# Performance work log

Measured on AMD Instinct MI355X. Metric: run time of the kernel, lower is better.

Reference implementation:

```python
import jax, jax.numpy as jnp
import numpy as np

# ---- Mamba2 hyperparameters (from init_kwargs + mamba_ssm defaults) ----
D_MODEL = 1024
D_STATE = 64
D_CONV = 4
EXPAND = 2
HEADDIM = 64                       # mamba_ssm default
D_INNER = EXPAND * D_MODEL         # 2048
NHEADS = D_INNER // HEADDIM        # 32
CONV_DIM = D_INNER + 2 * D_STATE   # 2176 (ngroups=1)
D_IN_PROJ = 2 * D_INNER + 2 * D_STATE + NHEADS  # 4256
CHUNK = 64                         # SSD chunk length
EPS = 1e-5


def segsum(x):
    """Stable segment-sum: out[..., i, j] = sum_{k=j+1..i} x[..., k] for i>=j, else -inf."""
    T = x.shape[-1]
    cs = jnp.cumsum(x, axis=-1)
    ss = cs[..., :, None] - cs[..., None, :]
    mask = jnp.tril(jnp.ones((T, T), dtype=bool))
    return jnp.where(mask, ss, -jnp.inf)


def setup_inputs() -> dict:
    key = jax.random.key(0)
    ks = jax.random.split(key, 8)
    x = jax.random.normal(ks[0], (2, 2048, D_MODEL), dtype=jnp.float32)
    ln_w = jnp.ones((D_MODEL,), jnp.float32)
    ln_b = jnp.zeros((D_MODEL,), jnp.float32)
    in_proj_w = jax.random.normal(ks[1], (D_MODEL, D_IN_PROJ), jnp.float32) * 0.02
    conv_w = jax.random.normal(ks[2], (CONV_DIM, D_CONV), jnp.float32) * 0.2
    conv_b = jnp.zeros((CONV_DIM,), jnp.float32)
    dt_bias = jax.random.normal(ks[3], (NHEADS,), jnp.float32) * 0.5
    A_log = jnp.log(jax.random.uniform(ks[4], (NHEADS,), jnp.float32, 1.0, 16.0))
    D = jnp.ones((NHEADS,), jnp.float32)
    norm_w = jnp.ones((D_INNER,), jnp.float32)
    out_proj_w = jax.random.normal(ks[5], (D_INNER, D_MODEL), jnp.float32) * 0.02
    return {"x": x, "ln_w": ln_w, "ln_b": ln_b, "in_proj_w": in_proj_w,
            "conv_w": conv_w, "conv_b": conv_b, "dt_bias": dt_bias,
            "A_log": A_log, "D": D, "norm_w": norm_w, "out_proj_w": out_proj_w}


def reference(x, ln_w, ln_b, in_proj_w, conv_w, conv_b, dt_bias, A_log, D,
              norm_w, out_proj_w):
    b, l, _ = x.shape
    # ---- pre-norm (LayerNorm) ----
    mu = jnp.mean(x, -1, keepdims=True)
    var = jnp.mean((x - mu) ** 2, -1, keepdims=True)
    h = (x - mu) * jax.lax.rsqrt(var + EPS) * ln_w + ln_b

    # ---- input projection & split ----
    zxbcdt = h @ in_proj_w                                   # (b,l,4256)
    z, xBC, dt = jnp.split(zxbcdt, [D_INNER, D_INNER + CONV_DIM], axis=-1)

    # ---- causal depthwise conv1d + SiLU ----
    xp = jnp.pad(xBC, ((0, 0), (D_CONV - 1, 0), (0, 0)))
    xconv = sum(xp[:, k:k + l, :] * conv_w[:, k] for k in range(D_CONV)) + conv_b
    xBC = jax.nn.silu(xconv)
    xs, B, C = jnp.split(xBC, [D_INNER, D_INNER + D_STATE], axis=-1)

    dt = jax.nn.softplus(dt + dt_bias)                       # (b,l,h)
    A = -jnp.exp(A_log)                                      # (h,)
    X = xs.reshape(b, l, NHEADS, HEADDIM)                    # (b,l,h,p)

    # ---- SSD chunked selective scan ----
    c = l // CHUNK
    X_dt = X * dt[..., None]
    A_dt = dt * A                                            # (b,l,h)
    Xc = X_dt.reshape(b, c, CHUNK, NHEADS, HEADDIM)          # (b,c,T,h,p)
    Ac = A_dt.reshape(b, c, CHUNK, NHEADS).transpose(0, 3, 1, 2)  # (b,h,c,T)
    Bc = B.reshape(b, c, CHUNK, D_STATE)                     # (b,c,T,n)
    Cc = C.reshape(b, c, CHUNK, D_STATE)

    A_cs = jnp.cumsum(Ac, axis=-1)                           # (b,h,c,T)
    Lmat = jnp.exp(segsum(Ac))                               # (b,h,c,T,T)
    Y_diag = jnp.einsum("bcln,bcsn,bhcls,bcshp->bclhp", Cc, Bc, Lmat, Xc)

    decay_states = jnp.exp(A_cs[..., -1:] - A_cs)            # (b,h,c,T)
    states = jnp.einsum("bcln,bhcl,bclhp->bchpn", Bc, decay_states, Xc)

    A_last = jnp.pad(A_cs[..., -1], ((0, 0), (0, 0), (1, 0)))
    decay_chunk = jnp.exp(segsum(A_last))                    # (b,h,c+1,c+1)
    states = jnp.concatenate([jnp.zeros_like(states[:, :1]), states], axis=1)
    states = jnp.einsum("bhzc,bchpn->bzhpn", decay_chunk, states)[:, :-1]

    Y_off = jnp.einsum("bcln,bchpn,bhcl->bclhp", Cc, states, jnp.exp(A_cs))
    Y = (Y_diag + Y_off).reshape(b, l, NHEADS, HEADDIM)

    # ---- D skip, gated RMSNorm, output projection ----
    Y = Y + X * D[None, None, :, None]
    y = Y.reshape(b, l, D_INNER)
    y = y * jax.nn.silu(z)
    y = y * jax.lax.rsqrt(jnp.mean(y * y, -1, keepdims=True) + EPS) * norm_w
    out = y @ out_proj_w

    return x + out  # residual
```

## Files before the change

kernel.cpp:

```cpp
#include <hip/hip_runtime.h>
#include <hip/hip_bf16.h>

#define BATCH   2
#define SEQ     2048
#define DMODEL  1024
#define DINNER  2048
#define DSTATE  64
#define NHEADS  32
#define HEADDIM 64
#define CONVDIM 2176
#define DINPROJ 4256
#define NPAD    4352
#define NCHUNK  32
#define EPSF    1e-5f
#define SP      88

typedef __bf16 bf16;
typedef bf16  bf16x8 __attribute__((ext_vector_type(8)));
typedef float f32x4  __attribute__((ext_vector_type(4)));

__device__ __forceinline__ void gll16(const bf16* g, bf16* l) {
    __builtin_amdgcn_global_load_lds(
        (const __attribute__((address_space(1))) void*)g,
        (__attribute__((address_space(3))) void*)l, 16, 0, 0);
}

__global__ __launch_bounds__(256) void ln_kernel(
    const float* __restrict__ x, const float* __restrict__ w,
    const float* __restrict__ bv, bf16* __restrict__ h) {
    int row = blockIdx.x;
    const float* xr = x + (size_t)row * DMODEL;
    bf16* hr = h + (size_t)row * DMODEL;
    int t = threadIdx.x;
    float4 v = ((const float4*)xr)[t];
    float s  = v.x + v.y + v.z + v.w;
    float ss = v.x*v.x + v.y*v.y + v.z*v.z + v.w*v.w;
    for (int o = 32; o > 0; o >>= 1) { s += __shfl_down(s, o); ss += __shfl_down(ss, o); }
    __shared__ float red[2][4];
    int wid = t >> 6, lane = t & 63;
    if (lane == 0) { red[0][wid] = s; red[1][wid] = ss; }
    __syncthreads();
    if (t == 0) {
        float a = 0, b2 = 0;
        for (int i = 0; i < 4; i++) { a += red[0][i]; b2 += red[1][i]; }
        red[0][0] = a; red[1][0] = b2;
    }
    __syncthreads();
    float mean = red[0][0] * (1.f / DMODEL);
    float var  = red[1][0] * (1.f / DMODEL) - mean * mean;
    float rstd = rsqrtf(var + EPSF);
    for (int i = t; i < DMODEL; i += 256)
        hr[i] = (bf16)((xr[i] - mean) * rstd * w[i] + bv[i]);
}

__global__ __launch_bounds__(256) void cvt_w_kernel(
    const float* __restrict__ W, bf16* __restrict__ Bt, int K, int N, int NP) {
    __shared__ float sm[32][33];
    int n0 = blockIdx.x * 32, k0 = blockIdx.y * 32;
    int tx = threadIdx.x & 31, ty = threadIdx.x >> 5;
    for (int i = 0; i < 4; i++) {
        int k = k0 + ty + i * 8, n = n0 + tx;
        sm[ty + i * 8][tx] = (n < N) ? W[(size_t)k * N + n] : 0.f;
    }
    __syncthreads();
    for (int i = 0; i < 4; i++) {
        int n = n0 + ty + i * 8, k = k0 + tx;
        if (n < NP) Bt[(size_t)n * K + k] = (bf16)sm[tx][ty + i * 8];
    }
}

template<int BM, int BN, typename OUT_T>
__global__ __launch_bounds__(256) void gemm_bf16_pipe(
    const bf16* __restrict__ A, const bf16* __restrict__ Bt,
    OUT_T* __restrict__ C, int M, int N, int K,
    const float* __restrict__ resid) {
    constexpr int MR = BM / 32;
    constexpr int NR = BN / 32;
    __shared__ __align__(16) bf16 sA[2][BM * 32];
    __shared__ __align__(16) bf16 sB[2][BN * 32];
    int t = threadIdx.x;
    int lane = t & 63, w = t >> 6;
    int m0 = blockIdx.y * BM, n0 = blockIdx.x * BN;
    int wm = w >> 1, wn = w & 1;
    f32x4 acc[MR][NR] = {};
    int srow = w * 16 + (lane >> 2);
    int scol = (lane & 3) * 8;
    int fr = lane & 15;
    int fc = (lane >> 4) * 8;
    auto stage = [&](int buf, int k0) {
        #pragma unroll
        for (int i = 0; i < BM / 64; i++)
            gll16(&A[(size_t)(m0 + i * 64 + srow) * K + k0 + scol],
                  &sA[buf][(i * 64 + w * 16) * 32]);
        #pragma unroll
        for (int i = 0; i < BN / 64; i++)
            gll16(&Bt[(size_t)(n0 + i * 64 + srow) * K + k0 + scol],
                  &sB[buf][(i * 64 + w * 16) * 32]);
    };
    int nt = K / 32;
    stage(0, 0);
    __syncthreads();
    int cur = 0;
    for (int tt = 0; tt < nt; tt++) {
        if (tt + 1 < nt) stage(cur ^ 1, (tt + 1) * 32);
        bf16x8 af[MR], bfr[NR];
        #pragma unroll
        for (int i = 0; i < MR; i++)
            af[i] = *(const bf16x8*)&sA[cur][(wm * (BM/2) + i * 16 + fr) * 32 + fc];
        #pragma unroll
        for (int j = 0; j < NR; j++)
            bfr[j] = *(const bf16x8*)&sB[cur][(wn * (BN/2) + j * 16 + fr) * 32 + fc];
        #pragma unroll
        for (int i = 0; i < MR; i++)
            #pragma unroll
            for (int j = 0; j < NR; j++)
                acc[i][j] = __builtin_amdgcn_mfma_f32_16x16x32_bf16(
                    af[i], bfr[j], acc[i][j], 0, 0, 0);
        __syncthreads();
        cur ^= 1;
    }
    #pragma unroll
    for (int i = 0; i < MR; i++) {
        #pragma unroll
        for (int j = 0; j < NR; j++) {
            int col = n0 + wn * (BN/2) + j * 16 + (lane & 15);
            #pragma unroll
            for (int r = 0; r < 4; r++) {
                int row = m0 + wm * (BM/2) + i * 16 + (lane >> 4) * 4 + r;
                float v = acc[i][j][r];
                if (resid) v += resid[(size_t)row * N + col];
                C[(size_t)row * N + col] = (OUT_T)v;
            }
        }
    }
}

__global__ __launch_bounds__(256) void conv_kernel(
    const bf16* __restrict__ zx, const float* __restrict__ cw,
    const float* __restrict__ cb, bf16* __restrict__ xs,
    bf16* __restrict__ Bm, bf16* __restrict__ Cm) {
    int idx = blockIdx.x * 256 + threadIdx.x;
    int ch = idx % CONVDIM;
    int bl = idx / CONVDIM;
    int b = bl / SEQ, tt = bl % SEQ;
    float acc = cb[ch];
    #pragma unroll
    for (int k = 0; k < 4; k++) {
        int tp = tt - 3 + k;
        if (tp >= 0)
            acc += (float)zx[(size_t)(b * SEQ + tp) * NPAD + DINNER + ch] * cw[ch * 4 + k];
    }
    float s = acc / (1.f + expf(-acc));
    if (ch < DINNER)              xs[(size_t)bl * DINNER + ch] = (bf16)s;
    else if (ch < DINNER+DSTATE)  Bm[bl * DSTATE + (ch - DINNER)] = (bf16)s;
    else                          Cm[bl * DSTATE + (ch - DINNER - DSTATE)] = (bf16)s;
}

__global__ __launch_bounds__(256) void dt_kernel(
    const bf16* __restrict__ zx, const float* __restrict__ dt_bias,
    float* __restrict__ dtb) {
    int idx = blockIdx.x * 256 + threadIdx.x;
    int hh = idx % NHEADS;
    int bl = idx / NHEADS;
    float v = (float)zx[(size_t)bl * NPAD + (DINNER + CONVDIM) + hh] + dt_bias[hh];
    dtb[idx] = (v > 20.f) ? v : log1pf(expf(v));
}

__global__ __launch_bounds__(256) void ssd_states_kernel(
    const bf16* __restrict__ xs, const bf16* __restrict__ Bm,
    const float* __restrict__ dtb, const float* __restrict__ A_log,
    float* __restrict__ states, float* __restrict__ Acs_g) {
    int blk = blockIdx.x;
    int hh = blk % NHEADS;
    int bc = blk / NHEADS;
    int c = bc % NCHUNK, b = bc / NCHUNK;
    __shared__ __align__(16) bf16 sXT[64 * SP];
    __shared__ __align__(16) bf16 sBT[64 * SP];
    __shared__ float dts[64], acs[64];
    int t = threadIdx.x;
    float Ah = -expf(A_log[hh]);
    if (t < 64) {
        float dv = dtb[(b * SEQ + c * 64 + t) * NHEADS + hh];
        float v = dv * Ah;
        #pragma unroll
        for (int o = 1; o < 64; o <<= 1) {
            float p = __shfl_up(v, o);
            if (t >= o) v += p;
        }
        dts[t] = dv; acs[t] = v;
        Acs_g[((b * NHEADS + hh) * NCHUNK + c) * 64 + t] = v;
    }
    __syncthreads();
    float alast = acs[63];
    {
        int l = t >> 2, c0 = (t & 3) * 16;
        int row = b * SEQ + c * 64 + l;
        float dl = dts[l];
        float wl = expf(alast - acs[l]);
        bf16x8 xv0 = *(const bf16x8*)&xs[(size_t)row * DINNER + hh * 64 + c0];
        bf16x8 xv1 = *(const bf16x8*)&xs[(size_t)row * DINNER + hh * 64 + c0 + 8];
        bf16x8 bv0 = *(const bf16x8*)&Bm[(size_t)row * DSTATE + c0];
        bf16x8 bv1 = *(const bf16x8*)&Bm[(size_t)row * DSTATE + c0 + 8];
        #pragma unroll
        for (int i = 0; i < 8; i++) {
            sXT[(c0 + i) * SP + l]     = (bf16)((float)xv0[i] * dl);
            sXT[(c0 + 8 + i) * SP + l] = (bf16)((float)xv1[i] * dl);
            sBT[(c0 + i) * SP + l]     = (bf16)((float)bv0[i] * wl);
            sBT[(c0 + 8 + i) * SP + l] = (bf16)((float)bv1[i] * wl);
        }
    }
    __syncthreads();
    int lane = t & 63, w = t >> 6;
    int wm = w >> 1, wn = w & 1;
    int fr = lane & 15, fc = (lane >> 4) * 8;
    f32x4 acc[2][2] = {};
    #pragma unroll
    for (int kk = 0; kk < 2; kk++) {
        bf16x8 a[2], bb[2];
        #pragma unroll
        for (int i = 0; i < 2; i++)
            a[i] = *(const bf16x8*)&sXT[(wm * 32 + i * 16 + fr) * SP + kk * 32 + fc];
        #pragma unroll
        for (int j = 0; j < 2; j++)
            bb[j] = *(const bf16x8*)&sBT[(wn * 32 + j * 16 + fr) * SP + kk * 32 + fc];
        #pragma unroll
        for (int i = 0; i < 2; i++)
            #pragma unroll
            for (int j = 0; j < 2; j++)
                acc[i][j] = __builtin_amdgcn_mfma_f32_16x16x32_bf16(
                    a[i], bb[j], acc[i][j], 0, 0, 0);
    }
    float* outp = states + (size_t)blk * 4096;
    #pragma unroll
    for (int i = 0; i < 2; i++)
        #pragma unroll
        for (int j = 0; j < 2; j++)
            #pragma unroll
            for (int r = 0; r < 4; r++)
                outp[(wm*32 + i*16 + (lane>>4)*4 + r) * 64 + wn*32 + j*16 + (lane&15)]
                    = acc[i][j][r];
}

__global__ __launch_bounds__(256) void ssd_scan_kernel(
    float* __restrict__ states, const float* __restrict__ Acs_g) {
    int bid = blockIdx.x;
    int slice = bid & 7, bh = bid >> 3;
    int hh = bh % NHEADS, b = bh / NHEADS;
    int e0 = slice * 512 + threadIdx.x * 2;
    float2 loc[NCHUNK];
    float dec[NCHUNK];
    #pragma unroll
    for (int c = 0; c < NCHUNK; c++) {
        loc[c] = *(const float2*)&states[(size_t)((b*NCHUNK+c)*NHEADS+hh)*4096 + e0];
        dec[c] = expf(Acs_g[((b*NHEADS+hh)*NCHUNK + c)*64 + 63]);
    }
    float2 S = make_float2(0.f, 0.f);
    #pragma unroll
    for (int c = 0; c < NCHUNK; c++) {
        float2 l = loc[c];
        *(float2*)&states[(size_t)((b*NCHUNK+c)*NHEADS+hh)*4096 + e0] = S;
        S.x = dec[c]*S.x + l.x;
        S.y = dec[c]*S.y + l.y;
    }
}

__global__ __launch_bounds__(256) void ssd_out_kernel(
    const bf16* __restrict__ xs, const bf16* __restrict__ Bm,
    const bf16* __restrict__ Cm, const float* __restrict__ dtb,
    const float* __restrict__ states, const float* __restrict__ Acs_g,
    const float* __restrict__ Dv, float* __restrict__ Y) {
    int blk = blockIdx.x;
    int hh = blk % NHEADS;
    int bc = blk / NHEADS;
    int c = bc % NCHUNK, b = bc / NCHUNK;
    __shared__ __align__(16) bf16 sC [64 * SP];
    __shared__ __align__(16) bf16 sBG[64 * SP];
    __shared__ __align__(16) bf16 sXS[64 * SP];
    __shared__ float acs[64], dts[64];
    int t = threadIdx.x;
    float4 sreg[4];
    {
        const float* sp = states + (size_t)blk * 4096 + t * 16;
        #pragma unroll
        for (int i = 0; i < 4; i++) sreg[i] = *(const float4*)&sp[i * 4];
    }
    if (t < 64) {
        acs[t] = Acs_g[((b * NHEADS + hh) * NCHUNK + c) * 64 + t];
        dts[t] = dtb[(b * SEQ + c * 64 + t) * NHEADS + hh];
    }
    {
        int l = t >> 2, c0 = (t & 3) * 16;
        int row = b * SEQ + c * 64 + l;
        *(bf16x8*)&sC[l * SP + c0]      = *(const bf16x8*)&Cm[(size_t)row * DSTATE + c0];
        *(bf16x8*)&sC[l * SP + c0 + 8]  = *(const bf16x8*)&Cm[(size_t)row * DSTATE + c0 + 8];
        *(bf16x8*)&sBG[l * SP + c0]     = *(const bf16x8*)&Bm[(size_t)row * DSTATE + c0];
        *(bf16x8*)&sBG[l * SP + c0 + 8] = *(const bf16x8*)&Bm[(size_t)row * DSTATE + c0 + 8];
        bf16x8 xv0 = *(const bf16x8*)&xs[(size_t)row * DINNER + hh * 64 + c0];
        bf16x8 xv1 = *(const bf16x8*)&xs[(size_t)row * DINNER + hh * 64 + c0 + 8];
        #pragma unroll
        for (int i = 0; i < 8; i++) {
            sXS[(c0 + i) * SP + l]     = xv0[i];
            sXS[(c0 + 8 + i) * SP + l] = xv1[i];
        }
    }
    __syncthreads();
    int lane = t & 63, w = t >> 6;
    int wm = w >> 1, wn = w & 1;
    int fr = lane & 15, fc = (lane >> 4) * 8;
    f32x4 g[2][2] = {};
    #pragma unroll
    for (int kk = 0; kk < 2; kk++) {
        bf16x8 a[2], bb[2];
        #pragma unroll
        for (int i = 0; i < 2; i++)
            a[i] = *(const bf16x8*)&sC[(wm * 32 + i * 16 + fr) * SP + kk * 32 + fc];
        #pragma unroll
        for (int j = 0; j < 2; j++)
            bb[j] = *(const bf16x8*)&sBG[(wn * 32 + j * 16 + fr) * SP + kk * 32 + fc];
        #pragma unroll
        for (int i = 0; i < 2; i++)
            #pragma unroll
            for (int j = 0; j < 2; j++)
                g[i][j] = __builtin_amdgcn_mfma_f32_16x16x32_bf16(a[i], bb[j], g[i][j], 0, 0, 0);
    }
    __syncthreads();
    #pragma unroll
    for (int i = 0; i < 2; i++) {
        #pragma unroll
        for (int j = 0; j < 2; j++) {
            int s = wn * 32 + j * 16 + (lane & 15);
            #pragma unroll
            for (int r = 0; r < 4; r++) {
                int l = wm * 32 + i * 16 + (lane >> 4) * 4 + r;
                float val = (s <= l) ? g[i][j][r] * expf(acs[l] - acs[s]) * dts[s] : 0.f;
                sBG[l * SP + s] = (bf16)val;
            }
        }
    }
    __syncthreads();
    f32x4 yd[2][2] = {};
    #pragma unroll
    for (int kk = 0; kk < 2; kk++) {
        bf16x8 a[2], bb[2];
        #pragma unroll
        for (int i = 0; i < 2; i++)
            a[i] = *(const bf16x8*)&sBG[(wm * 32 + i * 16 + fr) * SP + kk * 32 + fc];
        #pragma unroll
        for (int j = 0; j < 2; j++)
            bb[j] = *(const bf16x8*)&sXS[(wn * 32 + j * 16 + fr) * SP + kk * 32 + fc];
        #pragma unroll
        for (int i = 0; i < 2; i++)
            #pragma unroll
            for (int j = 0; j < 2; j++)
                yd[i][j] = __builtin_amdgcn_mfma_f32_16x16x32_bf16(a[i], bb[j], yd[i][j], 0, 0, 0);
    }
    float xk[2][2][4];
    #pragma unroll
    for (int i = 0; i < 2; i++)
        #pragma unroll
        for (int j = 0; j < 2; j++) {
            int p = wn * 32 + j * 16 + (lane & 15);
            #pragma unroll
            for (int r = 0; r < 4; r++) {
                int l = wm * 32 + i * 16 + (lane >> 4) * 4 + r;
                xk[i][j][r] = (float)sXS[p * SP + l];
            }
        }
    __syncthreads();
    {
        int p = t >> 2, n0 = (t & 3) * 16;
        const float* f = (const float*)sreg;
        bf16x8 s0, s1;
        #pragma unroll
        for (int q = 0; q < 8; q++) { s0[q] = (bf16)f[q]; s1[q] = (bf16)f[q + 8]; }
        *(bf16x8*)&sXS[p * SP + n0]     = s0;
        *(bf16x8*)&sXS[p * SP + n0 + 8] = s1;
    }
    __syncthreads();
    f32x4 yo[2][2] = {};
    #pragma unroll
    for (int kk = 0; kk < 2; kk++) {
        bf16x8 a[2], bb[2];
        #pragma unroll
        for (int i = 0; i < 2; i++)
            a[i] = *(const bf16x8*)&sC[(wm * 32 + i * 16 + fr) * SP + kk * 32 + fc];
        #pragma unroll
        for (int j = 0; j < 2; j++)
            bb[j] = *(const bf16x8*)&sXS[(wn * 32 + j * 16 + fr) * SP + kk * 32 + fc];
        #pragma unroll
        for (int i = 0; i < 2; i++)
            #pragma unroll
            for (int j = 0; j < 2; j++)
                yo[i][j] = __builtin_amdgcn_mfma_f32_16x16x32_bf16(a[i], bb[j], yo[i][j], 0, 0, 0);
    }
    float Dh = Dv[hh];
    #pragma unroll
    for (int i = 0; i < 2; i++) {
        #pragma unroll
        for (int j = 0; j < 2; j++) {
            int p = wn * 32 + j * 16 + (lane & 15);
            #pragma unroll
            for (int r = 0; r < 4; r++) {
                int l = wm * 32 + i * 16 + (lane >> 4) * 4 + r;
                int row = b * SEQ + c * 64 + l;
                Y[(size_t)row * DINNER + hh * 64 + p] =
                    yd[i][j][r] + expf(acs[l]) * yo[i][j][r] + Dh * xk[i][j][r];
            }
        }
    }
}

__global__ __launch_bounds__(256) void rms_kernel(
    const float* __restrict__ Y, const bf16* __restrict__ zx,
    const float* __restrict__ nw, bf16* __restrict__ yn) {
    int row = blockIdx.x;
    const float* yr = Y + (size_t)row * DINNER;
    const bf16* zr = zx + (size_t)row * NPAD;
    bf16* outr = yn + (size_t)row * DINNER;
    int t = threadIdx.x;
    float vals[8];
    float ss = 0.f;
    #pragma unroll
    for (int i = 0; i < 8; i++) {
        int idx = t + i * 256;
        float z = (float)zr[idx];
        float v = yr[idx] * (z / (1.f + expf(-z)));
        vals[i] = v;
        ss += v * v;
    }
    for (int o = 32; o > 0; o >>= 1) ss += __shfl_down(ss, o);
    __shared__ float red[4];
    int wid = t >> 6, lane = t & 63;
    if (lane == 0) red[wid] = ss;
    __syncthreads();
    if (t == 0) { float a = 0; for (int i = 0; i < 4; i++) a += red[i]; red[0] = a; }
    __syncthreads();
    float r = rsqrtf(red[0] * (1.f / DINNER) + EPSF);
    #pragma unroll
    for (int i = 0; i < 8; i++) {
        int idx = t + i * 256;
        outr[idx] = (bf16)(vals[i] * r * nw[idx]);
    }
}

extern "C" void kernel_launch(void* const* d_in, const int* in_sizes, int n_in,
                              void* d_out, int out_size, void* d_ws, size_t ws_size,
                              hipStream_t stream) {
    const float* x          = (const float*)d_in[0];
    const float* ln_w       = (const float*)d_in[1];
    const float* ln_b       = (const float*)d_in[2];
    const float* in_proj_w  = (const float*)d_in[3];
    const float* conv_w     = (const float*)d_in[4];
    const float* conv_b     = (const float*)d_in[5];
    const float* dt_bias    = (const float*)d_in[6];
    const float* A_log      = (const float*)d_in[7];
    const float* Dv         = (const float*)d_in[8];
    const float* norm_w     = (const float*)d_in[9];
    const float* out_proj_w = (const float*)d_in[10];
    float* out = (float*)d_out;

    char* ws = (char*)d_ws;
    size_t off = 0;
    auto alloc = [&](size_t bytes) { char* p = ws + off; off += (bytes + 255) & ~(size_t)255; return p; };
    bf16*  h_bf  = (bf16*) alloc((size_t)4096 * DMODEL * 2);
    bf16*  zx    = (bf16*) alloc((size_t)4096 * NPAD * 2);
    bf16*  xs    = (bf16*) alloc((size_t)4096 * DINNER * 2);
    float* states= (float*)alloc((size_t)2048 * 4096 * 4);
    float* Yb    = (float*)alloc((size_t)4096 * DINNER * 4);
    bf16*  Bt1   = (bf16*) alloc((size_t)NPAD * DMODEL * 2);
    float* dtb   = (float*)alloc((size_t)4096 * NHEADS * 4);
    float* Acs   = (float*)alloc((size_t)2 * NHEADS * NCHUNK * 64 * 4);
    bf16* Bm = h_bf;
    bf16* Cm = h_bf + (size_t)4096 * DSTATE;
    bf16* Bt2 = Bt1;
    bf16* yn = xs;

    ln_kernel<<<BATCH * SEQ, 256, 0, stream>>>(x, ln_w, ln_b, h_bf);

    {
        dim3 g(NPAD / 32, DMODEL / 32);
        cvt_w_kernel<<<g, 256, 0, stream>>>(in_proj_w, Bt1, DMODEL, DINPROJ, NPAD);
    }
    {
        dim3 g(NPAD / 128, (BATCH * SEQ) / 128);
        gemm_bf16_pipe<128, 128, bf16><<<g, 256, 0, stream>>>(
            h_bf, Bt1, zx, BATCH * SEQ, NPAD, DMODEL, nullptr);
    }

    conv_kernel<<<(BATCH * SEQ * CONVDIM) / 256, 256, 0, stream>>>(
        zx, conv_w, conv_b, xs, Bm, Cm);

    dt_kernel<<<(BATCH * SEQ * NHEADS) / 256, 256, 0, stream>>>(zx, dt_bias, dtb);

    ssd_states_kernel<<<BATCH * NCHUNK * NHEADS, 256, 0, stream>>>(
        xs, Bm, dtb, A_log, states, Acs);

    ssd_scan_kernel<<<BATCH * NHEADS * 8, 256, 0, stream>>>(states, Acs);

    ssd_out_kernel<<<BATCH * NCHUNK * NHEADS, 256, 0, stream>>>(
        xs, Bm, Cm, dtb, states, Acs, Dv, Yb);

    rms_kernel<<<BATCH * SEQ, 256, 0, stream>>>(Yb, zx, norm_w, yn);

    {
        dim3 g(DMODEL / 32, DINNER / 32);
        cvt_w_kernel<<<g, 256, 0, stream>>>(out_proj_w, Bt2, DINNER, DMODEL, DMODEL);
    }
    {
        dim3 g(DMODEL / 64, (BATCH * SEQ) / 128);
        gemm_bf16_pipe<128, 64, float><<<g, 256, 0, stream>>>(
            yn, Bt2, out, BATCH * SEQ, DMODEL, DINNER, x);
    }
}
```

Before: 219.6 us.

## Store SSD states and Y in bf16, merge weight-convert and conv/dt kernels

Both weight transpose/convert passes now run in a single launch at the start, with separate buffers for the two weights. The dt softplus is folded into the conv kernel. The inter-chunk states and the pre-norm Y are stored in bf16 instead of fp32, which halves the global traffic for the state scan, the output kernel and the RMS norm. The scan now processes four elements per thread. Together these cut launch count and memory bandwidth, at the cost of extra rounding error in the states and Y.

After: 206.9 us. 5.8% less time.

```diff
diff --git a/kernel.cpp b/kernel.cpp
--- a/kernel.cpp
+++ b/kernel.cpp
@@ -14,8 +14,10 @@
 #define NCHUNK  32
 #define EPSF    1e-5f
 #define SP      88
+#define CDT     (CONVDIM + NHEADS)
 
 typedef __bf16 bf16;
+typedef bf16  bf16x4 __attribute__((ext_vector_type(4)));
 typedef bf16  bf16x8 __attribute__((ext_vector_type(8)));
 typedef float f32x4  __attribute__((ext_vector_type(4)));
 
@@ -53,10 +55,21 @@
         hr[i] = (bf16)((xr[i] - mean) * rstd * w[i] + bv[i]);
 }
 
-__global__ __launch_bounds__(256) void cvt_w_kernel(
-    const float* __restrict__ W, bf16* __restrict__ Bt, int K, int N, int NP) {
+__global__ __launch_bounds__(256) void cvt_w_both_kernel(
+    const float* __restrict__ W1, const float* __restrict__ W2,
+    bf16* __restrict__ Bt1, bf16* __restrict__ Bt2) {
     __shared__ float sm[32][33];
-    int n0 = blockIdx.x * 32, k0 = blockIdx.y * 32;
+    int bid = blockIdx.x;
+    const float* W; bf16* Bt; int K, N, NP, bx, by;
+    if (bid < 4352) {
+        W = W1; Bt = Bt1; K = 1024; N = 4256; NP = 4352;
+        bx = bid % 136; by = bid / 136;
+    } else {
+        int b2 = bid - 4352;
+        W = W2; Bt = Bt2; K = 2048; N = 1024; NP = 1024;
+        bx = b2 % 32; by = b2 / 32;
+    }
+    int n0 = bx * 32, k0 = by * 32;
     int tx = threadIdx.x & 31, ty = threadIdx.x >> 5;
     for (int i = 0; i < 4; i++) {
         int k = k0 + ty + i * 8, n = n0 + tx;
@@ -135,13 +148,20 @@
     }
 }
 
-__global__ __launch_bounds__(256) void conv_kernel(
+__global__ __launch_bounds__(256) void convdt_kernel(
     const bf16* __restrict__ zx, const float* __restrict__ cw,
-    const float* __restrict__ cb, bf16* __restrict__ xs,
-    bf16* __restrict__ Bm, bf16* __restrict__ Cm) {
+    const float* __restrict__ cb, const float* __restrict__ dt_bias,
+    bf16* __restrict__ xs, bf16* __restrict__ Bm, bf16* __restrict__ Cm,
+    float* __restrict__ dtb) {
     int idx = blockIdx.x * 256 + threadIdx.x;
-    int ch = idx % CONVDIM;
-    int bl = idx / CONVDIM;
+    int ch = idx % CDT;
+    int bl = idx / CDT;
+    if (ch >= CONVDIM) {
+        int hh = ch - CONVDIM;
+        float v = (float)zx[(size_t)bl * NPAD + DINNER + ch] + dt_bias[hh];
+        dtb[bl * NHEADS + hh] = (v > 20.f) ? v : log1pf(expf(v));
+        return;
+    }
     int b = bl / SEQ, tt = bl % SEQ;
     float acc = cb[ch];
     #pragma unroll
@@ -156,20 +176,10 @@
     else                          Cm[bl * DSTATE + (ch - DINNER - DSTATE)] = (bf16)s;
 }
 
-__global__ __launch_bounds__(256) void dt_kernel(
-    const bf16* __restrict__ zx, const float* __restrict__ dt_bias,
-    float* __restrict__ dtb) {
-    int idx = blockIdx.x * 256 + threadIdx.x;
-    int hh = idx % NHEADS;
-    int bl = idx / NHEADS;
-    float v = (float)zx[(size_t)bl * NPAD + (DINNER + CONVDIM) + hh] + dt_bias[hh];
-    dtb[idx] = (v > 20.f) ? v : log1pf(expf(v));
-}
-
 __global__ __launch_bounds__(256) void ssd_states_kernel(
     const bf16* __restrict__ xs, const bf16* __restrict__ Bm,
     const float* __restrict__ dtb, const float* __restrict__ A_log,
-    float* __restrict__ states, float* __restrict__ Acs_g) {
+    bf16* __restrict__ states, float* __restrict__ Acs_g) {
     int blk = blockIdx.x;
     int hh = blk % NHEADS;
     int bc = blk / NHEADS;
@@ -230,7 +240,7 @@
                 acc[i][j] = __builtin_amdgcn_mfma_f32_16x16x32_bf16(
                     a[i], bb[j], acc[i][j], 0, 0, 0);
     }
-    float* outp = states + (size_t)blk * 4096;
+    bf16* outp = states + (size_t)blk * 4096;
     #pragma unroll
     for (int i = 0; i < 2; i++)
         #pragma unroll
@@ -238,37 +248,40 @@
             #pragma unroll
             for (int r = 0; r < 4; r++)
                 outp[(wm*32 + i*16 + (lane>>4)*4 + r) * 64 + wn*32 + j*16 + (lane&15)]
-                    = acc[i][j][r];
+                    = (bf16)acc[i][j][r];
 }
 
 __global__ __launch_bounds__(256) void ssd_scan_kernel(
-    float* __restrict__ states, const float* __restrict__ Acs_g) {
+    bf16* __restrict__ states, const float* __restrict__ Acs_g) {
     int bid = blockIdx.x;
-    int slice = bid & 7, bh = bid >> 3;
+    int slice = bid & 3, bh = bid >> 2;
     int hh = bh % NHEADS, b = bh / NHEADS;
-    int e0 = slice * 512 + threadIdx.x * 2;
-    float2 loc[NCHUNK];
+    int e0 = slice * 1024 + threadIdx.x * 4;
+    bf16x4 loc[NCHUNK];
     float dec[NCHUNK];
     #pragma unroll
     for (int c = 0; c < NCHUNK; c++) {
-        loc[c] = *(const float2*)&states[(size_t)((b*NCHUNK+c)*NHEADS+hh)*4096 + e0];
+        loc[c] = *(const bf16x4*)&states[(size_t)((b*NCHUNK+c)*NHEADS+hh)*4096 + e0];
         dec[c] = expf(Acs_g[((b*NHEADS+hh)*NCHUNK + c)*64 + 63]);
     }
-    float2 S = make_float2(0.f, 0.f);
+    float S0 = 0.f, S1 = 0.f, S2 = 0.f, S3 = 0.f;
     #pragma unroll
     for (int c = 0; c < NCHUNK; c++) {
-        float2 l = loc[c];
-        *(float2*)&states[(size_t)((b*NCHUNK+c)*NHEADS+hh)*4096 + e0] = S;
-        S.x = dec[c]*S.x + l.x;
-        S.y = dec[c]*S.y + l.y;
+        bf16x4 l = loc[c];
+        bf16x4 o; o[0] = (bf16)S0; o[1] = (bf16)S1; o[2] = (bf16)S2; o[3] = (bf16)S3;
+        *(bf16x4*)&states[(size_t)((b*NCHUNK+c)*NHEADS+hh)*4096 + e0] = o;
+        S0 = dec[c]*S0 + (float)l[0];
+        S1 = dec[c]*S1 + (float)l[1];
+        S2 = dec[c]*S2 + (float)l[2];
+        S3 = dec[c]*S3 + (float)l[3];
     }
 }
 
 __global__ __launch_bounds__(256) void ssd_out_kernel(
     const bf16* __restrict__ xs, const bf16* __restrict__ Bm,
     const bf16* __restrict__ Cm, const float* __restrict__ dtb,
-    const float* __restrict__ states, const float* __restrict__ Acs_g,
-    const float* __restrict__ Dv, float* __restrict__ Y) {
+    const bf16* __restrict__ states, const float* __restrict__ Acs_g,
+    const float* __restrict__ Dv, bf16* __restrict__ Y) {
     int blk = blockIdx.x;
     int hh = blk % NHEADS;
     int bc = blk / NHEADS;
@@ -278,11 +291,11 @@
     __shared__ __align__(16) bf16 sXS[64 * SP];
     __shared__ float acs[64], dts[64];
     int t = threadIdx.x;
-    float4 sreg[4];
+    bf16x8 sreg0, sreg1;
     {
-        const float* sp = states + (size_t)blk * 4096 + t * 16;
-        #pragma unroll
-        for (int i = 0; i < 4; i++) sreg[i] = *(const float4*)&sp[i * 4];
+        const bf16* sp = states + (size_t)blk * 4096 + t * 16;
+        sreg0 = *(const bf16x8*)&sp[0];
+        sreg1 = *(const bf16x8*)&sp[8];
     }
     if (t < 64) {
         acs[t] = Acs_g[((b * NHEADS + hh) * NCHUNK + c) * 64 + t];
@@ -369,12 +382,8 @@
     __syncthreads();
     {
         int p = t >> 2, n0 = (t & 3) * 16;
-        const float* f = (const float*)sreg;
-        bf16x8 s0, s1;
-        #pragma unroll
-        for (int q = 0; q < 8; q++) { s0[q] = (bf16)f[q]; s1[q] = (bf16)f[q + 8]; }
-        *(bf16x8*)&sXS[p * SP + n0]     = s0;
-        *(bf16x8*)&sXS[p * SP + n0 + 8] = s1;
+        *(bf16x8*)&sXS[p * SP + n0]     = sreg0;
+        *(bf16x8*)&sXS[p * SP + n0 + 8] = sreg1;
     }
     __syncthreads();
     f32x4 yo[2][2] = {};
@@ -404,17 +413,17 @@
                 int l = wm * 32 + i * 16 + (lane >> 4) * 4 + r;
                 int row = b * SEQ + c * 64 + l;
                 Y[(size_t)row * DINNER + hh * 64 + p] =
-                    yd[i][j][r] + expf(acs[l]) * yo[i][j][r] + Dh * xk[i][j][r];
+                    (bf16)(yd[i][j][r] + expf(acs[l]) * yo[i][j][r] + Dh * xk[i][j][r]);
             }
         }
     }
 }
 
 __global__ __launch_bounds__(256) void rms_kernel(
-    const float* __restrict__ Y, const bf16* __restrict__ zx,
+    const bf16* __restrict__ Y, const bf16* __restrict__ zx,
     const float* __restrict__ nw, bf16* __restrict__ yn) {
     int row = blockIdx.x;
-    const float* yr = Y + (size_t)row * DINNER;
+    const bf16* yr = Y + (size_t)row * DINNER;
     const bf16* zr = zx + (size_t)row * NPAD;
     bf16* outr = yn + (size_t)row * DINNER;
     int t = threadIdx.x;
@@ -424,7 +433,7 @@
     for (int i = 0; i < 8; i++) {
         int idx = t + i * 256;
         float z = (float)zr[idx];
-        float v = yr[idx] * (z / (1.f + expf(-z)));
+        float v = (float)yr[idx] * (z / (1.f + expf(-z)));
         vals[i] = v;
         ss += v * v;
     }
@@ -465,47 +474,39 @@
     bf16*  h_bf  = (bf16*) alloc((size_t)4096 * DMODEL * 2);
     bf16*  zx    = (bf16*) alloc((size_t)4096 * NPAD * 2);
     bf16*  xs    = (bf16*) alloc((size_t)4096 * DINNER * 2);
-    float* states= (float*)alloc((size_t)2048 * 4096 * 4);
-    float* Yb    = (float*)alloc((size_t)4096 * DINNER * 4);
+    bf16*  states= (bf16*) alloc((size_t)2048 * 4096 * 2);
+    bf16*  Yb    = (bf16*) alloc((size_t)4096 * DINNER * 2);
     bf16*  Bt1   = (bf16*) alloc((size_t)NPAD * DMODEL * 2);
+    bf16*  Bt2   = (bf16*) alloc((size_t)DMODEL * DINNER * 2);
     float* dtb   = (float*)alloc((size_t)4096 * NHEADS * 4);
     float* Acs   = (float*)alloc((size_t)2 * NHEADS * NCHUNK * 64 * 4);
     bf16* Bm = h_bf;
     bf16* Cm = h_bf + (size_t)4096 * DSTATE;
-    bf16* Bt2 = Bt1;
     bf16* yn = xs;
 
+    cvt_w_both_kernel<<<4352 + 2048, 256, 0, stream>>>(in_proj_w, out_proj_w, Bt1, Bt2);
+
     ln_kernel<<<BATCH * SEQ, 256, 0, stream>>>(x, ln_w, ln_b, h_bf);
 
-    {
-        dim3 g(NPAD / 32, DMODEL / 32);
-        cvt_w_kernel<<<g, 256, 0, stream>>>(in_proj_w, Bt1, DMODEL, DINPROJ, NPAD);
-    }
     {
         dim3 g(NPAD / 128, (BATCH * SEQ) / 128);
         gemm_bf16_pipe<128, 128, bf16><<<g, 256, 0, stream>>>(
             h_bf, Bt1, zx, BATCH * SEQ, NPAD, DMODEL, nullptr);
     }
 
-    conv_kernel<<<(BATCH * SEQ * CONVDIM) / 256, 256, 0, stream>>>(
-        zx, conv_w, conv_b, xs, Bm, Cm);
-
-    dt_kernel<<<(BATCH * SEQ * NHEADS) / 256, 256, 0, stream>>>(zx, dt_bias, dtb);
+    convdt_kernel<<<(BATCH * SEQ * CDT) / 256, 256, 0, stream>>>(
+        zx, conv_w, conv_b, dt_bias, xs, Bm, Cm, dtb);
 
     ssd_states_kernel<<<BATCH * NCHUNK * NHEADS, 256, 0, stream>>>(
         xs, Bm, dtb, A_log, states, Acs);
 
-    ssd_scan_kernel<<<BATCH * NHEADS * 8, 256, 0, stream>>>(states, Acs);
+    ssd_scan_kernel<<<BATCH * NHEADS * 4, 256, 0, stream>>>(states, Acs);
 
     ssd_out_kernel<<<BATCH * NCHUNK * NHEADS, 256, 0, stream>>>(
         xs, Bm, Cm, dtb, states, Acs, Dv, Yb);
 
     rms_kernel<<<BATCH * SEQ, 256, 0, stream>>>(Yb, zx, norm_w, yn);
 
-    {
-        dim3 g(DMODEL / 32, DINNER / 32);
-        cvt_w_kernel<<<g, 256, 0, stream>>>(out_proj_w, Bt2, DINNER, DMODEL, DMODEL);
-    }
     {
         dim3 g(DMODEL / 64, (BATCH * SEQ) / 128);
         gemm_bf16_pipe<128, 64, float><<<g, 256, 0, stream>>>(
```
